# Kernel tuning notes

Measured on AMD Instinct MI355X. Metric: run time of the kernel, lower is better.

Reference implementation:

```python
import jax, jax.numpy as jnp
import numpy as np

F_FACETS = 400000
TEX_PER = 4            # textures per facet (counts sum must equal total textures)
T_TEX = F_FACETS * TEX_PER
C_IN = 64
C_OUT = 64
L = 2
N_BASIS = (L + 1) ** 2  # 9
BN_EPS = 1e-3


def setup_inputs() -> dict:
    key = jax.random.key(0)
    k1, k2, k3 = jax.random.split(key, 3)
    input_texture = jax.random.normal(k1, (T_TEX, C_IN), jnp.float32)
    bary_coeff = jax.random.uniform(k2, (T_TEX, N_BASIS), jnp.float32)
    # per-facet texture counts; constant 4 so counts sum exactly to T_TEX
    num_texture = jnp.full((F_FACETS,), TEX_PER, dtype=jnp.int32)
    # xavier_normal_ on [O, I, K]: fan_in = I*K, fan_out = ... torch uses fan_in=I*K? For 3D it treats dim1*rest.
    std = float(np.sqrt(2.0 / (C_IN * N_BASIS + C_OUT * N_BASIS)))
    weights = jax.random.normal(k3, (C_OUT, C_IN, N_BASIS), jnp.float32) * std
    biases = jnp.zeros((1, C_OUT), jnp.float32)
    gamma = jnp.ones((C_OUT,), jnp.float32)
    beta = jnp.zeros((C_OUT,), jnp.float32)
    return {
        "input_texture": input_texture,
        "bary_coeff": bary_coeff,
        "weights": weights,
        "biases": biases,
        "gamma": gamma,
        "beta": beta,
        "num_texture": num_texture,
    }


def reference(input_texture, bary_coeff, weights, biases, gamma, beta, num_texture):
    T = input_texture.shape[0]
    n_facets = num_texture.shape[0]
    n_basis = weights.shape[2]
    # per-texture contribution: contrib[t,o] = sum_{i,k} x[t,i] * W[o,i,k] * bary[t,k]
    # loop over small fixed basis count (9) to avoid a [T, I, K] intermediate
    contrib = jnp.zeros((T, weights.shape[0]), dtype=input_texture.dtype)
    for k in range(n_basis):
        contrib = contrib + (input_texture @ weights[:, :, k].T) * bary_coeff[:, k:k + 1]
    # scatter-sum per facet (ragged groups given by num_texture), then average
    seg_ids = jnp.repeat(jnp.arange(n_facets), num_texture, total_repeat_length=T)
    facet_sum = jax.ops.segment_sum(contrib, seg_ids, num_segments=n_facets)
    out = facet_sum / num_texture[:, None].astype(facet_sum.dtype)
    # bias + ReLU
    out = jax.nn.relu(out + biases)
    # BatchNorm1d in training mode: batch stats (biased variance), eps=1e-3
    mu = jnp.mean(out, axis=0)
    var = jnp.mean(jnp.square(out - mu), axis=0)
    out = (out - mu) * jax.lax.rsqrt(var + BN_EPS) * gamma + beta
    return out
```

## Files before the change

### kernel.cpp

```cpp
#include <hip/hip_runtime.h>


typedef _Float16 half8  __attribute__((ext_vector_type(8)));
typedef _Float16 h2     __attribute__((ext_vector_type(2)));
typedef __fp16   fp16x2 __attribute__((ext_vector_type(2)));
typedef float    f32x4  __attribute__((ext_vector_type(4)));

#define NGROUPS 100000
#define NPAIRS  50000
#define FFACETS 400000
#define GRID1   768
#define LDSP    9472

#define WAITV(N) asm volatile("s_waitcnt vmcnt(" #N ")" ::: "memory")
#define FENCE()  asm volatile("" ::: "memory")

union H8 { h2 h[4]; half8 v; };

static __device__ __forceinline__ h2 pkrtz(float a, float b) {
    fp16x2 r = __builtin_amdgcn_cvt_pkrtz(a, b);
    return __builtin_bit_cast(h2, r);
}

static __device__ __forceinline__ float qsum(float s) {
    s += __builtin_bit_cast(float, __builtin_amdgcn_mov_dpp(
             __builtin_bit_cast(int, s), 0xB1, 0xF, 0xF, true));
    s += __builtin_bit_cast(float, __builtin_amdgcn_mov_dpp(
             __builtin_bit_cast(int, s), 0x4E, 0xF, 0xF, true));
    return s;
}

static __device__ __forceinline__ void gload16(const void* g, void* l) {
    __builtin_amdgcn_global_load_lds((const __attribute__((address_space(1))) void*)g,
                                     (__attribute__((address_space(3))) void*)l, 16, 0, 0);
}

__global__ __launch_bounds__(256) void prep_kernel(const float* __restrict__ W,
                                                   _Float16* __restrict__ wswz,
                                                   float* __restrict__ stats) {
    int idx = blockIdx.x * 256 + threadIdx.x;
    if (idx < 36864) {
        int j    = idx & 7;
        int lane = (idx >> 3) & 63;
        int mt   = (idx >> 9) & 3;
        int c    = idx >> 11;
        int o    = mt * 16 + (lane & 15);
        int i    = (c & 1) * 32 + ((lane >> 4) << 3) + j;
        int kb   = c >> 1;
        wswz[idx] = (_Float16)W[(o * 64 + i) * 9 + kb];
    }
    if (idx < 128) stats[idx] = 0.0f;
}

__global__ __launch_bounds__(256, 3) void pass1_kernel(
    const float* __restrict__ X, const float* __restrict__ BARY,
    const _Float16* __restrict__ WSWZ, const float* __restrict__ BIAS,
    const int* __restrict__ NTEX, float* __restrict__ OUT,
    float* __restrict__ stats) {

    __shared__ __align__(16) char ldsbuf[3 * LDSP];
    __shared__ float sl_s[64];
    __shared__ float sl_s2[64];

    const int tid  = threadIdx.x;
    const int wave = tid >> 6;
    const int lane = tid & 63;
    const int col  = lane & 15;
    const int quad = lane >> 4;

    half8 wf[18];
#pragma unroll
    for (int c = 0; c < 18; ++c)
        wf[c] = *(const half8*)(WSWZ + ((size_t)(c * 4 + wave) * 64 + lane) * 8);

    const f32x4 biasv = *(const f32x4*)(BIAS + wave * 16 + quad * 4);

    const int xdst = (wave << 10) + (lane << 4);
    const int xsrc = ((lane & 15) << 8) + ((lane >> 4) << 5)
                   + ((wave & 1) << 4) + ((wave >> 1) << 7);
    const char* Xb  = (const char*)X;
    const char* BAb = (const char*)BARY;
    const char* NTb = (const char*)NTEX;

    const int xrd = lane << 4;
    const int bco = 8192 + col * 36;
    const int nco = 9344 + ((col >> 2) << 2);

    float sacc[4]  = {0.f, 0.f, 0.f, 0.f};
    float s2acc[4] = {0.f, 0.f, 0.f, 0.f};

    const int b = blockIdx.x;
    const int n = (NPAIRS - 1 - b) / GRID1 + 1;

    auto STAGE = [&](char* S, int u) {
        const char* xs = Xb + (size_t)u * 8192;
        FENCE();
        gload16(xs + xsrc,        S + xdst);
        gload16(xs + 4096 + xsrc, S + 4096 + xdst);
        gload16(BAb + (size_t)u * 1152 + lane * 16, S + 8192 + lane * 16);
        if (lane < 8) gload16(BAb + (size_t)u * 1152 + 1024 + lane * 16, S + 9216 + lane * 16);
        if (lane < 2) gload16(NTb + (size_t)u * 32 + lane * 16,          S + 9344 + lane * 16);
        FENCE();
    };

    auto EPI = [&](f32x4 acc, float rc, int f) {
        f32x4 vv;
#pragma unroll
        for (int r = 0; r < 4; ++r) {
            float s = qsum(acc[r]);
            s = s * rc + biasv[r];
            s = s > 0.f ? s : 0.f;
            vv[r] = s;
            sacc[r]  += s;
            s2acc[r] += s * s;
        }
        if ((col & 3) == 0)
            *(f32x4*)(OUT + (size_t)f * 64 + wave * 16 + quad * 4) = vv;
    };

    auto ITER = [&](const char* L, char* S, int u, int upre, bool do_stage) {
        __builtin_amdgcn_s_barrier();
        FENCE();
        f32x4 r0[4], r1[4];
#pragma unroll
        for (int j = 0; j < 4; ++j) {
            r0[j] = *(const f32x4*)(L + (j << 10) + xrd);
            r1[j] = *(const f32x4*)(L + 4096 + (j << 10) + xrd);
        }
        float bF0[9], bF1[9];
#pragma unroll
        for (int k = 0; k < 9; ++k) bF0[k] = *(const float*)(L + bco + k * 4);
#pragma unroll
        for (int k = 0; k < 9; ++k) bF1[k] = *(const float*)(L + bco + 576 + k * 4);
        const int nt0 = *(const int*)(L + nco);
        const int nt1 = *(const int*)(L + nco + 16);

        if (do_stage) STAGE(S, upre);

        h2 xh0[8], xh1[8], bh0[9], bh1[9];
        xh0[0] = pkrtz(r0[0][0], r0[0][1]);  xh0[1] = pkrtz(r0[0][2], r0[0][3]);
        xh0[2] = pkrtz(r0[1][0], r0[1][1]);  xh0[3] = pkrtz(r0[1][2], r0[1][3]);
        xh0[4] = pkrtz(r0[2][0], r0[2][1]);  xh0[5] = pkrtz(r0[2][2], r0[2][3]);
        xh0[6] = pkrtz(r0[3][0], r0[3][1]);  xh0[7] = pkrtz(r0[3][2], r0[3][3]);
        xh1[0] = pkrtz(r1[0][0], r1[0][1]);  xh1[1] = pkrtz(r1[0][2], r1[0][3]);
        xh1[2] = pkrtz(r1[1][0], r1[1][1]);  xh1[3] = pkrtz(r1[1][2], r1[1][3]);
        xh1[4] = pkrtz(r1[2][0], r1[2][1]);  xh1[5] = pkrtz(r1[2][2], r1[2][3]);
        xh1[6] = pkrtz(r1[3][0], r1[3][1]);  xh1[7] = pkrtz(r1[3][2], r1[3][3]);
#pragma unroll
        for (int k = 0; k < 9; ++k) { bh0[k] = pkrtz(bF0[k], bF0[k]); bh1[k] = pkrtz(bF1[k], bF1[k]); }
        const float rc0 = __builtin_amdgcn_rcpf((float)nt0);
        const float rc1 = __builtin_amdgcn_rcpf((float)nt1);

        f32x4 accA = {0.f, 0.f, 0.f, 0.f};
        f32x4 accB = {0.f, 0.f, 0.f, 0.f};
        __builtin_amdgcn_s_setprio(1);
#pragma unroll
        for (int c = 0; c < 18; ++c) {
            const int hh = (c & 1) * 4;
            const h2 bkA = bh0[c >> 1];
            const h2 bkB = bh1[c >> 1];
            H8 fa, fb;
            fa.h[0] = xh0[hh + 0] * bkA;  fa.h[1] = xh0[hh + 1] * bkA;
            fa.h[2] = xh0[hh + 2] * bkA;  fa.h[3] = xh0[hh + 3] * bkA;
            accA = __builtin_amdgcn_mfma_f32_16x16x32_f16(wf[c], fa.v, accA, 0, 0, 0);
            fb.h[0] = xh1[hh + 0] * bkB;  fb.h[1] = xh1[hh + 1] * bkB;
            fb.h[2] = xh1[hh + 2] * bkB;  fb.h[3] = xh1[hh + 3] * bkB;
            accB = __builtin_amdgcn_mfma_f32_16x16x32_f16(wf[c], fb.v, accB, 0, 0, 0);
        }
        __builtin_amdgcn_s_setprio(0);

        const int f0 = u * 8 + (col >> 2);
        EPI(accA, rc0, f0);
        EPI(accB, rc1, f0 + 4);
    };

    char* B0 = ldsbuf;
    char* B1 = ldsbuf + LDSP;
    char* B2 = ldsbuf + 2 * LDSP;

    STAGE(B0, b);
    STAGE(B1, b + GRID1);
    WAITV(5); ITER(B0, B2, b,         b + 2 * GRID1, true);
    WAITV(7); ITER(B1, B0, b + GRID1, b + 3 * GRID1, true);
    char *rd = B2, *st = B1, *ot = B0;
    int t = 2;
    for (; t < n - 2; ++t) {
        WAITV(9);
        ITER(rd, st, b + t * GRID1, b + (t + 2) * GRID1, true);
        char* tmp = ot; ot = st; st = rd; rd = tmp;
    }
    WAITV(9); ITER(rd, st, b + t * GRID1, 0, false);
    { char* tmp = ot; ot = st; st = rd; rd = tmp; } ++t;
    WAITV(4); ITER(rd, st, b + t * GRID1, 0, false);

#pragma unroll
    for (int r = 0; r < 4; ++r) {
        float s = sacc[r], s2 = s2acc[r];
        s  += __shfl_xor(s, 1);  s  += __shfl_xor(s, 2);
        s  += __shfl_xor(s, 4);  s  += __shfl_xor(s, 8);
        s2 += __shfl_xor(s2, 1); s2 += __shfl_xor(s2, 2);
        s2 += __shfl_xor(s2, 4); s2 += __shfl_xor(s2, 8);
        if (col == 0) {
            sl_s [wave * 16 + quad * 4 + r] = s  * 0.25f;
            sl_s2[wave * 16 + quad * 4 + r] = s2 * 0.25f;
        }
    }
    __syncthreads();
    if (tid < 64)        atomicAdd(&stats[tid],      sl_s [tid]);
    else if (tid < 128)  atomicAdd(&stats[tid],      sl_s2[tid - 64]);
}

__global__ __launch_bounds__(256) void pass3_kernel(float* __restrict__ OUT,
    const float* __restrict__ stats, const float* __restrict__ gamma,
    const float* __restrict__ beta) {
    const int tid = threadIdx.x;
    const size_t l = (size_t)blockIdx.x * 256 + tid;
    const int c0 = ((int)l & 15) * 4;
    float mu[4], sc[4], be[4];
    const float invF = 1.0f / (float)FFACETS;
#pragma unroll
    for (int u = 0; u < 4; ++u) {
        int ch = c0 + u;
        float m  = stats[ch] * invF;
        float va = stats[64 + ch] * invF - m * m;
        mu[u] = m;
        sc[u] = rsqrtf(va + 1e-3f) * gamma[ch];
        be[u] = beta[ch];
    }
    const size_t n4 = (size_t)FFACETS * 16;
    for (size_t i = l; i < n4; i += (size_t)gridDim.x * 256) {
        f32x4 v = ((f32x4*)OUT)[i];
#pragma unroll
        for (int u = 0; u < 4; ++u)
            v[u] = (v[u] - mu[u]) * sc[u] + be[u];
        ((f32x4*)OUT)[i] = v;
    }
}

extern "C" void kernel_launch(void* const* d_in, const int* in_sizes, int n_in,
                              void* d_out, int out_size, void* d_ws, size_t ws_size,
                              hipStream_t stream) {
    const float* X     = (const float*)d_in[0];
    const float* BARY  = (const float*)d_in[1];
    const float* W     = (const float*)d_in[2];
    const float* BIAS  = (const float*)d_in[3];
    const float* GAMMA = (const float*)d_in[4];
    const float* BETA  = (const float*)d_in[5];
    const int*   NTEX  = (const int*)d_in[6];
    float* OUT = (float*)d_out;

    _Float16* wswz = (_Float16*)d_ws;
    float* stats   = (float*)((char*)d_ws + 73728);

    prep_kernel<<<144, 256, 0, stream>>>(W, wswz, stats);
    pass1_kernel<<<GRID1, 256, 0, stream>>>(X, BARY, wswz, BIAS, NTEX, OUT, stats);
    pass3_kernel<<<2048, 256, 0, stream>>>(OUT, stats, GAMMA, BETA);
}
```

Baseline: 665.9 us.

## Switch pass1 to 32x32x16 MFMA tiles processing 16 facets per block step

Restructures the main kernel to use 32x32x16 f16 MFMA instead of paired 16x16x32, with each wave covering 32 output channels by 32 textures and each block step handling 16 facets. The LDS staging buffers double in size, X rows are stored with an XOR swizzle to avoid bank conflicts, and bias moves into shared memory. Launch bounds drop to 2 blocks per CU and the grid shrinks, trading occupancy and register pressure (36 weight fragments held per wave) for fewer, larger matrix instructions and more data reuse per stage.

```diff
diff --git a/kernel.cpp b/kernel.cpp
--- a/kernel.cpp
+++ b/kernel.cpp
@@ -5,14 +5,15 @@
 typedef _Float16 h2     __attribute__((ext_vector_type(2)));
 typedef __fp16   fp16x2 __attribute__((ext_vector_type(2)));
 typedef float    f32x4  __attribute__((ext_vector_type(4)));
-
-#define NGROUPS 100000
-#define NPAIRS  50000
+typedef float    f32x16 __attribute__((ext_vector_type(16)));
+
+#define NQUADS  25000
 #define FFACETS 400000
-#define GRID1   768
-#define LDSP    9472
+#define GRID1   512
+#define LDSP    18752
 
 #define WAITV(N) asm volatile("s_waitcnt vmcnt(" #N ")" ::: "memory")
+#define WAITL0() asm volatile("s_waitcnt lgkmcnt(0)" ::: "memory")
 #define FENCE()  asm volatile("" ::: "memory")
 
 union H8 { h2 h[4]; half8 v; };
@@ -42,136 +43,152 @@
     if (idx < 36864) {
         int j    = idx & 7;
         int lane = (idx >> 3) & 63;
-        int mt   = (idx >> 9) & 3;
-        int c    = idx >> 11;
-        int o    = mt * 16 + (lane & 15);
-        int i    = (c & 1) * 32 + ((lane >> 4) << 3) + j;
-        int kb   = c >> 1;
+        int wc   = (idx >> 9) & 1;
+        int c    = idx >> 10;
+        int o    = wc * 32 + (lane & 31);
+        int i    = (c & 3) * 16 + (lane >> 5) * 8 + j;
+        int kb   = c >> 2;
         wswz[idx] = (_Float16)W[(o * 64 + i) * 9 + kb];
     }
     if (idx < 128) stats[idx] = 0.0f;
 }
 
-__global__ __launch_bounds__(256, 3) void pass1_kernel(
+__global__ __launch_bounds__(256, 2) void pass1_kernel(
     const float* __restrict__ X, const float* __restrict__ BARY,
     const _Float16* __restrict__ WSWZ, const float* __restrict__ BIAS,
     const int* __restrict__ NTEX, float* __restrict__ OUT,
     float* __restrict__ stats) {
 
     __shared__ __align__(16) char ldsbuf[3 * LDSP];
-    __shared__ float sl_s[64];
-    __shared__ float sl_s2[64];
+    __shared__ float sl_s[128];
+    __shared__ float sl_s2[128];
+    __shared__ float sbias[64];
 
     const int tid  = threadIdx.x;
     const int wave = tid >> 6;
     const int lane = tid & 63;
-    const int col  = lane & 15;
-    const int quad = lane >> 4;
-
-    half8 wf[18];
-#pragma unroll
-    for (int c = 0; c < 18; ++c)
-        wf[c] = *(const half8*)(WSWZ + ((size_t)(c * 4 + wave) * 64 + lane) * 8);
-
-    const f32x4 biasv = *(const f32x4*)(BIAS + wave * 16 + quad * 4);
-
-    const int xdst = (wave << 10) + (lane << 4);
-    const int xsrc = ((lane & 15) << 8) + ((lane >> 4) << 5)
-                   + ((wave & 1) << 4) + ((wave >> 1) << 7);
+    const int wc   = wave >> 1;
+    const int wt   = wave & 1;
+    const int t    = lane & 31;
+    const int hi   = lane >> 5;
+    const int q    = lane & 3;
+
+    sbias[lane] = BIAS[lane];
+    WAITL0();
+
+    half8 wf[36];
+#pragma unroll
+    for (int c = 0; c < 36; ++c)
+        wf[c] = *(const half8*)(WSWZ + ((size_t)(c * 2 + wc) * 64 + lane) * 8);
+
+    int xsg[4];
+#pragma unroll
+    for (int i = 0; i < 4; ++i) {
+        const int tt = wave * 16 + i * 4 + (lane >> 4);
+        xsg[i] = tt * 256 + (((lane & 15) ^ (tt & 15)) << 4);
+    }
+    const int xd = wave * 4096 + lane * 16;
     const char* Xb  = (const char*)X;
     const char* BAb = (const char*)BARY;
     const char* NTb = (const char*)NTEX;
 
-    const int xrd = lane << 4;
-    const int bco = 8192 + col * 36;
-    const int nco = 9344 + ((col >> 2) << 2);
+    int xr[8];
+#pragma unroll
+    for (int ciq = 0; ciq < 4; ++ciq)
+#pragma unroll
+        for (int jj = 0; jj < 2; ++jj)
+            xr[ciq * 2 + jj] = (wt * 32 + t) * 256 +
+                               (((ciq * 4 + hi * 2 + jj) ^ (lane & 15)) << 4);
+    const int bco = 16384 + (wt * 2 + (t >> 4)) * 576 + (lane & 15) * 36;
+    const int nco = 18688 + wt * 32 + ((t >> 2) << 2);
 
     float sacc[4]  = {0.f, 0.f, 0.f, 0.f};
     float s2acc[4] = {0.f, 0.f, 0.f, 0.f};
 
     const int b = blockIdx.x;
-    const int n = (NPAIRS - 1 - b) / GRID1 + 1;
+    const int n = (NQUADS - 1 - b) / GRID1 + 1;
 
     auto STAGE = [&](char* S, int u) {
-        const char* xs = Xb + (size_t)u * 8192;
+        const char* xs = Xb + (size_t)u * 16384;
         FENCE();
-        gload16(xs + xsrc,        S + xdst);
-        gload16(xs + 4096 + xsrc, S + 4096 + xdst);
-        gload16(BAb + (size_t)u * 1152 + lane * 16, S + 8192 + lane * 16);
-        if (lane < 8) gload16(BAb + (size_t)u * 1152 + 1024 + lane * 16, S + 9216 + lane * 16);
-        if (lane < 2) gload16(NTb + (size_t)u * 32 + lane * 16,          S + 9344 + lane * 16);
+        gload16(xs + xsg[0], S + xd);
+        gload16(xs + xsg[1], S + xd + 1024);
+        gload16(xs + xsg[2], S + xd + 2048);
+        gload16(xs + xsg[3], S + xd + 3072);
+        if (lane < 36) gload16(BAb + (size_t)u * 2304 + wave * 576 + lane * 16,
+                               S + 16384 + wave * 576 + lane * 16);
+        if (lane < 1)  gload16(NTb + (size_t)u * 64 + wave * 16, S + 18688 + wave * 16);
         FENCE();
-    };
-
-    auto EPI = [&](f32x4 acc, float rc, int f) {
-        f32x4 vv;
-#pragma unroll
-        for (int r = 0; r < 4; ++r) {
-            float s = qsum(acc[r]);
-            s = s * rc + biasv[r];
-            s = s > 0.f ? s : 0.f;
-            vv[r] = s;
-            sacc[r]  += s;
-            s2acc[r] += s * s;
-        }
-        if ((col & 3) == 0)
-            *(f32x4*)(OUT + (size_t)f * 64 + wave * 16 + quad * 4) = vv;
     };
 
     auto ITER = [&](const char* L, char* S, int u, int upre, bool do_stage) {
         __builtin_amdgcn_s_barrier();
         FENCE();
-        f32x4 r0[4], r1[4];
+        f32x4 r[8];
+#pragma unroll
+        for (int k = 0; k < 8; ++k) r[k] = *(const f32x4*)(L + xr[k]);
+        float bF[9];
+#pragma unroll
+        for (int k = 0; k < 9; ++k) bF[k] = *(const float*)(L + bco + k * 4);
+        const int nt = *(const int*)(L + nco);
+        f32x4 bias4[4];
+#pragma unroll
+        for (int qp = 0; qp < 4; ++qp)
+            bias4[qp] = *(const f32x4*)&sbias[wc * 32 + hi * 4 + qp * 8];
+
+        if (do_stage) STAGE(S, upre);
+
+        h2 xh[16], bh[9];
+#pragma unroll
+        for (int k = 0; k < 8; ++k) {
+            xh[k * 2]     = pkrtz(r[k][0], r[k][1]);
+            xh[k * 2 + 1] = pkrtz(r[k][2], r[k][3]);
+        }
+#pragma unroll
+        for (int k = 0; k < 9; ++k) bh[k] = pkrtz(bF[k], bF[k]);
+        const float rc = __builtin_amdgcn_rcpf((float)nt);
+
+        f32x16 acc = {};
+        __builtin_amdgcn_s_setprio(1);
+#pragma unroll
+        for (int c = 0; c < 36; ++c) {
+            const h2 bk = bh[c >> 2];
+            const int xb = (c & 3) * 4;
+            H8 bf;
+            bf.h[0] = xh[xb + 0] * bk;  bf.h[1] = xh[xb + 1] * bk;
+            bf.h[2] = xh[xb + 2] * bk;  bf.h[3] = xh[xb + 3] * bk;
+            acc = __builtin_amdgcn_mfma_f32_32x32x16_f16(wf[c], bf.v, acc, 0, 0, 0);
+        }
+        __builtin_amdgcn_s_setprio(0);
+
+        f32x4 vq[4];
+#pragma unroll
+        for (int qp = 0; qp < 4; ++qp)
+#pragma unroll
+            for (int j = 0; j < 4; ++j) {
+                float s = qsum(acc[qp * 4 + j]);
+                s = s * rc + bias4[qp][j];
+                vq[qp][j] = s > 0.f ? s : 0.f;
+            }
+
 #pragma unroll
         for (int j = 0; j < 4; ++j) {
-            r0[j] = *(const f32x4*)(L + (j << 10) + xrd);
-            r1[j] = *(const f32x4*)(L + 4096 + (j << 10) + xrd);
-        }
-        float bF0[9], bF1[9];
-#pragma unroll
-        for (int k = 0; k < 9; ++k) bF0[k] = *(const float*)(L + bco + k * 4);
-#pragma unroll
-        for (int k = 0; k < 9; ++k) bF1[k] = *(const float*)(L + bco + 576 + k * 4);
-        const int nt0 = *(const int*)(L + nco);
-        const int nt1 = *(const int*)(L + nco + 16);
-
-        if (do_stage) STAGE(S, upre);
-
-        h2 xh0[8], xh1[8], bh0[9], bh1[9];
-        xh0[0] = pkrtz(r0[0][0], r0[0][1]);  xh0[1] = pkrtz(r0[0][2], r0[0][3]);
-        xh0[2] = pkrtz(r0[1][0], r0[1][1]);  xh0[3] = pkrtz(r0[1][2], r0[1][3]);
-        xh0[4] = pkrtz(r0[2][0], r0[2][1]);  xh0[5] = pkrtz(r0[2][2], r0[2][3]);
-        xh0[6] = pkrtz(r0[3][0], r0[3][1]);  xh0[7] = pkrtz(r0[3][2], r0[3][3]);
-        xh1[0] = pkrtz(r1[0][0], r1[0][1]);  xh1[1] = pkrtz(r1[0][2], r1[0][3]);
-        xh1[2] = pkrtz(r1[1][0], r1[1][1]);  xh1[3] = pkrtz(r1[1][2], r1[1][3]);
-        xh1[4] = pkrtz(r1[2][0], r1[2][1]);  xh1[5] = pkrtz(r1[2][2], r1[2][3]);
-        xh1[6] = pkrtz(r1[3][0], r1[3][1]);  xh1[7] = pkrtz(r1[3][2], r1[3][3]);
-#pragma unroll
-        for (int k = 0; k < 9; ++k) { bh0[k] = pkrtz(bF0[k], bF0[k]); bh1[k] = pkrtz(bF1[k], bF1[k]); }
-        const float rc0 = __builtin_amdgcn_rcpf((float)nt0);
-        const float rc1 = __builtin_amdgcn_rcpf((float)nt1);
-
-        f32x4 accA = {0.f, 0.f, 0.f, 0.f};
-        f32x4 accB = {0.f, 0.f, 0.f, 0.f};
-        __builtin_amdgcn_s_setprio(1);
-#pragma unroll
-        for (int c = 0; c < 18; ++c) {
-            const int hh = (c & 1) * 4;
-            const h2 bkA = bh0[c >> 1];
-            const h2 bkB = bh1[c >> 1];
-            H8 fa, fb;
-            fa.h[0] = xh0[hh + 0] * bkA;  fa.h[1] = xh0[hh + 1] * bkA;
-            fa.h[2] = xh0[hh + 2] * bkA;  fa.h[3] = xh0[hh + 3] * bkA;
-            accA = __builtin_amdgcn_mfma_f32_16x16x32_f16(wf[c], fa.v, accA, 0, 0, 0);
-            fb.h[0] = xh1[hh + 0] * bkB;  fb.h[1] = xh1[hh + 1] * bkB;
-            fb.h[2] = xh1[hh + 2] * bkB;  fb.h[3] = xh1[hh + 3] * bkB;
-            accB = __builtin_amdgcn_mfma_f32_16x16x32_f16(wf[c], fb.v, accB, 0, 0, 0);
-        }
-        __builtin_amdgcn_s_setprio(0);
-
-        const int f0 = u * 8 + (col >> 2);
-        EPI(accA, rc0, f0);
-        EPI(accB, rc1, f0 + 4);
+            float p = vq[0][j];
+            p = (q == 1) ? vq[1][j] : p;
+            p = (q == 2) ? vq[2][j] : p;
+            p = (q == 3) ? vq[3][j] : p;
+            sacc[j]  += p;
+            s2acc[j] += p * p;
+        }
+
+        const int f = u * 16 + wt * 8 + (t >> 2);
+        if ((lane & 3) == 0) {
+            float* op = OUT + (size_t)f * 64 + wc * 32 + hi * 4;
+            *(f32x4*)(op)      = vq[0];
+            *(f32x4*)(op + 8)  = vq[1];
+            *(f32x4*)(op + 16) = vq[2];
+            *(f32x4*)(op + 24) = vq[3];
+        }
     };
 
     char* B0 = ldsbuf;
@@ -180,34 +197,33 @@
 
     STAGE(B0, b);
     STAGE(B1, b + GRID1);
-    WAITV(5); ITER(B0, B2, b,         b + 2 * GRID1, true);
-    WAITV(7); ITER(B1, B0, b + GRID1, b + 3 * GRID1, true);
+    WAITV(6);  ITER(B0, B2, b,         b + 2 * GRID1, true);
+    WAITV(10); ITER(B1, B0, b + GRID1, b + 3 * GRID1, true);
     char *rd = B2, *st = B1, *ot = B0;
-    int t = 2;
-    for (; t < n - 2; ++t) {
-        WAITV(9);
-        ITER(rd, st, b + t * GRID1, b + (t + 2) * GRID1, true);
+    int tI = 2;
+    for (; tI < n - 2; ++tI) {
+        WAITV(14);
+        ITER(rd, st, b + tI * GRID1, b + (tI + 2) * GRID1, true);
         char* tmp = ot; ot = st; st = rd; rd = tmp;
     }
-    WAITV(9); ITER(rd, st, b + t * GRID1, 0, false);
-    { char* tmp = ot; ot = st; st = rd; rd = tmp; } ++t;
-    WAITV(4); ITER(rd, st, b + t * GRID1, 0, false);
-
-#pragma unroll
-    for (int r = 0; r < 4; ++r) {
-        float s = sacc[r], s2 = s2acc[r];
-        s  += __shfl_xor(s, 1);  s  += __shfl_xor(s, 2);
-        s  += __shfl_xor(s, 4);  s  += __shfl_xor(s, 8);
-        s2 += __shfl_xor(s2, 1); s2 += __shfl_xor(s2, 2);
-        s2 += __shfl_xor(s2, 4); s2 += __shfl_xor(s2, 8);
-        if (col == 0) {
-            sl_s [wave * 16 + quad * 4 + r] = s  * 0.25f;
-            sl_s2[wave * 16 + quad * 4 + r] = s2 * 0.25f;
+    WAITV(14); ITER(rd, st, b + tI * GRID1, 0, false);
+    { char* tmp = ot; ot = st; st = rd; rd = tmp; } ++tI;
+    WAITV(8);  ITER(rd, st, b + tI * GRID1, 0, false);
+
+#pragma unroll
+    for (int j = 0; j < 4; ++j) {
+        float s = sacc[j], s2 = s2acc[j];
+        s  += __shfl_xor(s, 4);   s  += __shfl_xor(s, 8);   s  += __shfl_xor(s, 16);
+        s2 += __shfl_xor(s2, 4);  s2 += __shfl_xor(s2, 8);  s2 += __shfl_xor(s2, 16);
+        if (((lane >> 2) & 7) == 0) {
+            const int idx = wt * 64 + wc * 32 + hi * 4 + q * 8 + j;
+            sl_s[idx]  = s;
+            sl_s2[idx] = s2;
         }
     }
     __syncthreads();
-    if (tid < 64)        atomicAdd(&stats[tid],      sl_s [tid]);
-    else if (tid < 128)  atomicAdd(&stats[tid],      sl_s2[tid - 64]);
+    if (tid < 64)        atomicAdd(&stats[tid], sl_s[tid] + sl_s[tid + 64]);
+    else if (tid < 128)  atomicAdd(&stats[tid], sl_s2[tid - 64] + sl_s2[tid]);
 }
 
 __global__ __launch_bounds__(256) void pass3_kernel(float* __restrict__ OUT,
```

After: 653.3 us (median of 2 runs). Within noise of the previous version (-1.9%).
